# Kernel tuning notes

Measured on AMD Instinct MI355X. Metric: run time of the kernel, lower is better.

Reference implementation:

```python
import jax, jax.numpy as jnp
import numpy as np

N = 16384          # items per call
ITEM_NUM = 1_000_000
TAG_NUM = 100_000
D = 64             # embedding_size
T = 8              # max tags per item (padded)
H = 256            # item_tower hidden


def setup_inputs() -> dict:
    key = jax.random.key(0)
    ks = jax.random.split(key, 8)
    item_ids = jax.random.randint(ks[0], (N,), 0, ITEM_NUM + 1, dtype=jnp.int32)
    tag_ids = jax.random.randint(ks[1], (N, T), 0, TAG_NUM + 1, dtype=jnp.int32)
    tag_lens = jax.random.randint(ks[2], (N,), 1, T + 1, dtype=jnp.int32)  # >=1 tag, like the dataset
    item_table = jax.random.normal(ks[3], (ITEM_NUM + 1, D), jnp.float32) * 0.02
    item_dat_table = jax.random.normal(ks[4], (ITEM_NUM + 1, D), jnp.float32) * 0.02
    tag_table = jax.random.normal(ks[5], (TAG_NUM + 1, D), jnp.float32) * 0.02
    W1 = jax.random.normal(ks[6], (3 * D, H), jnp.float32) * 0.05
    b1 = jnp.zeros((H,), jnp.float32)
    W2 = jax.random.normal(ks[7], (H, D), jnp.float32) * 0.05
    b2 = jnp.zeros((D,), jnp.float32)
    return {"item_ids": item_ids, "tag_ids": tag_ids, "tag_lens": tag_lens,
            "item_table": item_table, "item_dat_table": item_dat_table,
            "tag_table": tag_table, "W1": W1, "b1": b1, "W2": W2, "b2": b2}


def reference(item_ids, tag_ids, tag_lens, item_table, item_dat_table, tag_table, W1, b1, W2, b2):
    # batched version of Model.items(): per-item embedding gathers,
    # ragged tag mean-pool, concat, 2-layer MLP tower.
    e_item = item_table[item_ids]                      # [N, D]
    e_dat = item_dat_table[item_ids]                   # [N, D]
    tag_e = tag_table[tag_ids]                         # [N, T, D]
    mask = (jnp.arange(T)[None, :] < tag_lens[:, None]).astype(tag_e.dtype)  # [N, T]
    tag_mean = (tag_e * mask[:, :, None]).sum(axis=1) / tag_lens[:, None].astype(tag_e.dtype)
    # tower_input = cat([item_emb, tag_mean, zeros_like(dat_emb)])
    x = jnp.concatenate([e_item, tag_mean, jnp.zeros_like(e_dat)], axis=-1)  # [N, 3D]
    h = jax.nn.relu(x @ W1 + b1)                       # [N, H]
    out = h @ W2 + b2                                  # [N, D]
    return out, e_dat
```

## Files before the change

### kernel.cpp

```cpp
#include <hip/hip_runtime.h>

#define N_ITEMS 16384
#define D 64
#define T 8
#define H 256

__global__ __launch_bounds__(256) void k_gather(
    const int* __restrict__ item_ids,
    const int* __restrict__ tag_ids,
    const int* __restrict__ tag_lens,
    const float* __restrict__ item_table,
    const float* __restrict__ item_dat_table,
    const float* __restrict__ tag_table,
    float* __restrict__ x,
    float* __restrict__ e_dat_out)
{
    const int wave = __builtin_amdgcn_readfirstlane(threadIdx.x >> 6);
    const int lane = threadIdx.x & 63;
    const int i = blockIdx.x * 4 + wave;

    const int id  = item_ids[i];
    const int len = tag_lens[i];

    const float e_it = item_table[(size_t)id * D + lane];
    const float e_da = item_dat_table[(size_t)id * D + lane];

    float s = 0.f;
#pragma unroll
    for (int t = 0; t < T; ++t) {
        if (t < len) {
            const int tg = tag_ids[i * T + t];
            s += tag_table[(size_t)tg * D + lane];
        }
    }

    x[i * 128 + lane]      = e_it;
    x[i * 128 + 64 + lane] = s / (float)len;
    e_dat_out[i * D + lane] = e_da;
}

__global__ __launch_bounds__(256) void k_layer1(
    const float* __restrict__ x,
    const float* __restrict__ W1,
    const float* __restrict__ b1,
    float* __restrict__ h)
{
    const int j  = threadIdx.x;
    const int i0 = blockIdx.x * 16;
    const float* xrow = x + (size_t)i0 * 128;

    float acc[16];
    const float bj = b1[j];
#pragma unroll
    for (int i = 0; i < 16; ++i) acc[i] = bj;

    for (int k = 0; k < 128; k += 4) {
        const float w0 = W1[(size_t)(k + 0) * H + j];
        const float w1 = W1[(size_t)(k + 1) * H + j];
        const float w2 = W1[(size_t)(k + 2) * H + j];
        const float w3 = W1[(size_t)(k + 3) * H + j];
#pragma unroll
        for (int i = 0; i < 16; ++i) {
            const float4 xv = *reinterpret_cast<const float4*>(xrow + i * 128 + k);
            acc[i] = fmaf(xv.x, w0, acc[i]);
            acc[i] = fmaf(xv.y, w1, acc[i]);
            acc[i] = fmaf(xv.z, w2, acc[i]);
            acc[i] = fmaf(xv.w, w3, acc[i]);
        }
    }

#pragma unroll
    for (int i = 0; i < 16; ++i)
        h[(size_t)(i0 + i) * H + j] = fmaxf(acc[i], 0.f);
}

__global__ __launch_bounds__(256) void k_layer2(
    const float* __restrict__ h,
    const float* __restrict__ W2,
    const float* __restrict__ b2,
    float* __restrict__ out)
{
    const int lane = threadIdx.x & 63;
    const int wave = __builtin_amdgcn_readfirstlane(threadIdx.x >> 6);
    const int i0   = blockIdx.x * 32 + wave * 8;
    const int j    = lane;
    const float* hrow = h + (size_t)i0 * H;

    float acc[8];
    const float bj = b2[j];
#pragma unroll
    for (int i = 0; i < 8; ++i) acc[i] = bj;

    for (int k = 0; k < 256; k += 4) {
        const float w0 = W2[(size_t)(k + 0) * 64 + j];
        const float w1 = W2[(size_t)(k + 1) * 64 + j];
        const float w2v = W2[(size_t)(k + 2) * 64 + j];
        const float w3 = W2[(size_t)(k + 3) * 64 + j];
#pragma unroll
        for (int i = 0; i < 8; ++i) {
            const float4 hv = *reinterpret_cast<const float4*>(hrow + i * H + k);
            acc[i] = fmaf(hv.x, w0, acc[i]);
            acc[i] = fmaf(hv.y, w1, acc[i]);
            acc[i] = fmaf(hv.z, w2v, acc[i]);
            acc[i] = fmaf(hv.w, w3, acc[i]);
        }
    }

#pragma unroll
    for (int i = 0; i < 8; ++i)
        out[(size_t)(i0 + i) * 64 + j] = acc[i];
}

extern "C" void kernel_launch(void* const* d_in, const int* in_sizes, int n_in,
                              void* d_out, int out_size, void* d_ws, size_t ws_size,
                              hipStream_t stream) {
    const int*   item_ids       = (const int*)d_in[0];
    const int*   tag_ids        = (const int*)d_in[1];
    const int*   tag_lens       = (const int*)d_in[2];
    const float* item_table     = (const float*)d_in[3];
    const float* item_dat_table = (const float*)d_in[4];
    const float* tag_table      = (const float*)d_in[5];
    const float* W1             = (const float*)d_in[6];
    const float* b1             = (const float*)d_in[7];
    const float* W2             = (const float*)d_in[8];
    const float* b2             = (const float*)d_in[9];

    float* out       = (float*)d_out;
    float* e_dat_out = out + (size_t)N_ITEMS * D;

    float* x = (float*)d_ws;
    float* h = x + (size_t)N_ITEMS * 128;

    k_gather<<<N_ITEMS / 4, 256, 0, stream>>>(item_ids, tag_ids, tag_lens,
                                              item_table, item_dat_table,
                                              tag_table, x, e_dat_out);
    k_layer1<<<N_ITEMS / 16, 256, 0, stream>>>(x, W1, b1, h);
    k_layer2<<<N_ITEMS / 32, 256, 0, stream>>>(h, W2, b2, out);
}
```

Measured before the change: 485.0 us.

## Fuse gather, layer1 and layer2 into one kernel with LDS-staged activations

Merges the three kernels into one that handles a 16-item tile per block. The gathered input and hidden activations stay in shared memory instead of making a round trip through global workspace, and two launches go away. Both matmuls are re-tiled so each thread computes float4 column groups with vectorized weight loads. The cost is that gather latency and compute now run in the same block separated by barriers, and the LDS footprint can limit occupancy.

```diff
diff --git a/kernel.cpp b/kernel.cpp
--- a/kernel.cpp
+++ b/kernel.cpp
@@ -4,111 +4,133 @@
 #define D 64
 #define T 8
 #define H 256
+#define TILE 16
+#define HS_STRIDE 260
 
-__global__ __launch_bounds__(256) void k_gather(
+__global__ __launch_bounds__(256) void k_fused(
     const int* __restrict__ item_ids,
     const int* __restrict__ tag_ids,
     const int* __restrict__ tag_lens,
     const float* __restrict__ item_table,
     const float* __restrict__ item_dat_table,
     const float* __restrict__ tag_table,
-    float* __restrict__ x,
+    const float* __restrict__ W1,
+    const float* __restrict__ b1,
+    const float* __restrict__ W2,
+    const float* __restrict__ b2,
+    float* __restrict__ out,
     float* __restrict__ e_dat_out)
 {
-    const int wave = __builtin_amdgcn_readfirstlane(threadIdx.x >> 6);
-    const int lane = threadIdx.x & 63;
-    const int i = blockIdx.x * 4 + wave;
+    __shared__ float xs[TILE * 128];
+    __shared__ float hs[TILE * HS_STRIDE];
 
-    const int id  = item_ids[i];
-    const int len = tag_lens[i];
+    const int tid  = threadIdx.x;
+    const int lane = tid & 63;
+    const int wave = tid >> 6;
+    const int i0   = blockIdx.x * TILE;
 
-    const float e_it = item_table[(size_t)id * D + lane];
-    const float e_da = item_dat_table[(size_t)id * D + lane];
+#pragma unroll
+    for (int r = 0; r < 4; ++r) {
+        const int il = wave * 4 + r;
+        const int gi = i0 + il;
+        const int id  = item_ids[gi];
+        const int len = tag_lens[gi];
 
-    float s = 0.f;
+        xs[il * 128 + lane]      = item_table[(size_t)id * D + lane];
+        e_dat_out[(size_t)gi * D + lane] = item_dat_table[(size_t)id * D + lane];
+
+        float s = 0.f;
 #pragma unroll
-    for (int t = 0; t < T; ++t) {
-        if (t < len) {
-            const int tg = tag_ids[i * T + t];
-            s += tag_table[(size_t)tg * D + lane];
+        for (int t = 0; t < T; ++t) {
+            if (t < len) {
+                const int tg = tag_ids[gi * T + t];
+                s += tag_table[(size_t)tg * D + lane];
+            }
+        }
+        xs[il * 128 + 64 + lane] = s / (float)len;
+    }
+    __syncthreads();
+
+    {
+        const int c = tid & 63;
+        const int g = tid >> 6;
+        float4 acc[4];
+        const float4 bj = *reinterpret_cast<const float4*>(b1 + 4 * c);
+#pragma unroll
+        for (int r = 0; r < 4; ++r) acc[r] = bj;
+
+        for (int k = 0; k < 128; k += 4) {
+            float4 xv[4];
+#pragma unroll
+            for (int r = 0; r < 4; ++r)
+                xv[r] = *reinterpret_cast<const float4*>(&xs[(g * 4 + r) * 128 + k]);
+            const float4 w0 = *reinterpret_cast<const float4*>(W1 + (size_t)(k + 0) * H + 4 * c);
+            const float4 w1 = *reinterpret_cast<const float4*>(W1 + (size_t)(k + 1) * H + 4 * c);
+            const float4 w2 = *reinterpret_cast<const float4*>(W1 + (size_t)(k + 2) * H + 4 * c);
+            const float4 w3 = *reinterpret_cast<const float4*>(W1 + (size_t)(k + 3) * H + 4 * c);
+#pragma unroll
+            for (int r = 0; r < 4; ++r) {
+                acc[r].x = fmaf(xv[r].x, w0.x, acc[r].x);
+                acc[r].y = fmaf(xv[r].x, w0.y, acc[r].y);
+                acc[r].z = fmaf(xv[r].x, w0.z, acc[r].z);
+                acc[r].w = fmaf(xv[r].x, w0.w, acc[r].w);
+                acc[r].x = fmaf(xv[r].y, w1.x, acc[r].x);
+                acc[r].y = fmaf(xv[r].y, w1.y, acc[r].y);
+                acc[r].z = fmaf(xv[r].y, w1.z, acc[r].z);
+                acc[r].w = fmaf(xv[r].y, w1.w, acc[r].w);
+                acc[r].x = fmaf(xv[r].z, w2.x, acc[r].x);
+                acc[r].y = fmaf(xv[r].z, w2.y, acc[r].y);
+                acc[r].z = fmaf(xv[r].z, w2.z, acc[r].z);
+                acc[r].w = fmaf(xv[r].z, w2.w, acc[r].w);
+                acc[r].x = fmaf(xv[r].w, w3.x, acc[r].x);
+                acc[r].y = fmaf(xv[r].w, w3.y, acc[r].y);
+                acc[r].z = fmaf(xv[r].w, w3.z, acc[r].z);
+                acc[r].w = fmaf(xv[r].w, w3.w, acc[r].w);
+            }
+        }
+#pragma unroll
+        for (int r = 0; r < 4; ++r) {
+            float4 hval;
+            hval.x = fmaxf(acc[r].x, 0.f);
+            hval.y = fmaxf(acc[r].y, 0.f);
+            hval.z = fmaxf(acc[r].z, 0.f);
+            hval.w = fmaxf(acc[r].w, 0.f);
+            *reinterpret_cast<float4*>(&hs[(g * 4 + r) * HS_STRIDE + 4 * c]) = hval;
         }
     }
+    __syncthreads();
 
-    x[i * 128 + lane]      = e_it;
-    x[i * 128 + 64 + lane] = s / (float)len;
-    e_dat_out[i * D + lane] = e_da;
-}
+    {
+        const int item = tid >> 4;
+        const int cg   = tid & 15;
+        float4 acc = *reinterpret_cast<const float4*>(b2 + 4 * cg);
+        const float* hrow = &hs[item * HS_STRIDE];
 
-__global__ __launch_bounds__(256) void k_layer1(
-    const float* __restrict__ x,
-    const float* __restrict__ W1,
-    const float* __restrict__ b1,
-    float* __restrict__ h)
-{
-    const int j  = threadIdx.x;
-    const int i0 = blockIdx.x * 16;
-    const float* xrow = x + (size_t)i0 * 128;
-
-    float acc[16];
-    const float bj = b1[j];
-#pragma unroll
-    for (int i = 0; i < 16; ++i) acc[i] = bj;
-
-    for (int k = 0; k < 128; k += 4) {
-        const float w0 = W1[(size_t)(k + 0) * H + j];
-        const float w1 = W1[(size_t)(k + 1) * H + j];
-        const float w2 = W1[(size_t)(k + 2) * H + j];
-        const float w3 = W1[(size_t)(k + 3) * H + j];
-#pragma unroll
-        for (int i = 0; i < 16; ++i) {
-            const float4 xv = *reinterpret_cast<const float4*>(xrow + i * 128 + k);
-            acc[i] = fmaf(xv.x, w0, acc[i]);
-            acc[i] = fmaf(xv.y, w1, acc[i]);
-            acc[i] = fmaf(xv.z, w2, acc[i]);
-            acc[i] = fmaf(xv.w, w3, acc[i]);
+        for (int k = 0; k < 256; k += 4) {
+            const float4 hv = *reinterpret_cast<const float4*>(&hrow[k]);
+            const float4 w0 = *reinterpret_cast<const float4*>(W2 + (size_t)(k + 0) * 64 + 4 * cg);
+            const float4 w1 = *reinterpret_cast<const float4*>(W2 + (size_t)(k + 1) * 64 + 4 * cg);
+            const float4 w2 = *reinterpret_cast<const float4*>(W2 + (size_t)(k + 2) * 64 + 4 * cg);
+            const float4 w3 = *reinterpret_cast<const float4*>(W2 + (size_t)(k + 3) * 64 + 4 * cg);
+            acc.x = fmaf(hv.x, w0.x, acc.x);
+            acc.y = fmaf(hv.x, w0.y, acc.y);
+            acc.z = fmaf(hv.x, w0.z, acc.z);
+            acc.w = fmaf(hv.x, w0.w, acc.w);
+            acc.x = fmaf(hv.y, w1.x, acc.x);
+            acc.y = fmaf(hv.y, w1.y, acc.y);
+            acc.z = fmaf(hv.y, w1.z, acc.z);
+            acc.w = fmaf(hv.y, w1.w, acc.w);
+            acc.x = fmaf(hv.z, w2.x, acc.x);
+            acc.y = fmaf(hv.z, w2.y, acc.y);
+            acc.z = fmaf(hv.z, w2.z, acc.z);
+            acc.w = fmaf(hv.z, w2.w, acc.w);
+            acc.x = fmaf(hv.w, w3.x, acc.x);
+            acc.y = fmaf(hv.w, w3.y, acc.y);
+            acc.z = fmaf(hv.w, w3.z, acc.z);
+            acc.w = fmaf(hv.w, w3.w, acc.w);
         }
+        *reinterpret_cast<float4*>(out + (size_t)(i0 + item) * 64 + 4 * cg) = acc;
     }
-
-#pragma unroll
-    for (int i = 0; i < 16; ++i)
-        h[(size_t)(i0 + i) * H + j] = fmaxf(acc[i], 0.f);
-}
-
-__global__ __launch_bounds__(256) void k_layer2(
-    const float* __restrict__ h,
-    const float* __restrict__ W2,
-    const float* __restrict__ b2,
-    float* __restrict__ out)
-{
-    const int lane = threadIdx.x & 63;
-    const int wave = __builtin_amdgcn_readfirstlane(threadIdx.x >> 6);
-    const int i0   = blockIdx.x * 32 + wave * 8;
-    const int j    = lane;
-    const float* hrow = h + (size_t)i0 * H;
-
-    float acc[8];
-    const float bj = b2[j];
-#pragma unroll
-    for (int i = 0; i < 8; ++i) acc[i] = bj;
-
-    for (int k = 0; k < 256; k += 4) {
-        const float w0 = W2[(size_t)(k + 0) * 64 + j];
-        const float w1 = W2[(size_t)(k + 1) * 64 + j];
-        const float w2v = W2[(size_t)(k + 2) * 64 + j];
-        const float w3 = W2[(size_t)(k + 3) * 64 + j];
-#pragma unroll
-        for (int i = 0; i < 8; ++i) {
-            const float4 hv = *reinterpret_cast<const float4*>(hrow + i * H + k);
-            acc[i] = fmaf(hv.x, w0, acc[i]);
-            acc[i] = fmaf(hv.y, w1, acc[i]);
-            acc[i] = fmaf(hv.z, w2v, acc[i]);
-            acc[i] = fmaf(hv.w, w3, acc[i]);
-        }
-    }
-
-#pragma unroll
-    for (int i = 0; i < 8; ++i)
-        out[(size_t)(i0 + i) * 64 + j] = acc[i];
 }
 
 extern "C" void kernel_launch(void* const* d_in, const int* in_sizes, int n_in,
@@ -128,12 +150,7 @@
     float* out       = (float*)d_out;
     float* e_dat_out = out + (size_t)N_ITEMS * D;
 
-    float* x = (float*)d_ws;
-    float* h = x + (size_t)N_ITEMS * 128;
-
-    k_gather<<<N_ITEMS / 4, 256, 0, stream>>>(item_ids, tag_ids, tag_lens,
-                                              item_table, item_dat_table,
-                                              tag_table, x, e_dat_out);
-    k_layer1<<<N_ITEMS / 16, 256, 0, stream>>>(x, W1, b1, h);
-    k_layer2<<<N_ITEMS / 32, 256, 0, stream>>>(h, W2, b2, out);
+    k_fused<<<N_ITEMS / TILE, 256, 0, stream>>>(item_ids, tag_ids, tag_lens,
+                                                item_table, item_dat_table, tag_table,
+                                                W1, b1, W2, b2, out, e_dat_out);
 }
```

New measurement: 474.1 us. 2.3% less time.
